# Kernel tuning notes

Measured on AMD Instinct MI355X. Metric: run time of the kernel, lower is better.

The kernel has to match this reference:

```python
import jax, jax.numpy as jnp
import numpy as np

N, E, DIN, HID, HEADS = 50000, 400000, 256, 64, 4
EPS_BN = 1e-5

def setup_inputs() -> dict:
    key = jax.random.key(0)
    ks = jax.random.split(key, 12)
    inp = {}
    inp['x'] = jax.random.normal(ks[0], (N, DIN), dtype=jnp.float32)
    inp['edge_index'] = jax.random.randint(ks[1], (2, E), 0, N, dtype=jnp.int64)
    s = 1.0 / np.sqrt(DIN)
    inp['W1'] = jax.random.uniform(ks[2], (DIN, HEADS * HID), jnp.float32, -s, s)
    inp['a_src1'] = jax.random.normal(ks[3], (HEADS, HID), dtype=jnp.float32) * 0.1
    inp['a_dst1'] = jax.random.normal(ks[4], (HEADS, HID), dtype=jnp.float32) * 0.1
    inp['b1'] = jnp.zeros((HEADS * HID,), jnp.float32)
    inp['bn1_w'] = jnp.ones((HEADS * HID,), jnp.float32)
    inp['bn1_b'] = jnp.zeros((HEADS * HID,), jnp.float32)
    inp['bn1_m'] = jnp.zeros((HEADS * HID,), jnp.float32)
    inp['bn1_v'] = jnp.ones((HEADS * HID,), jnp.float32)
    s2 = 1.0 / np.sqrt(HEADS * HID)
    inp['W2'] = jax.random.uniform(ks[5], (HEADS * HID, HID), jnp.float32, -s2, s2)
    inp['a_src2'] = jax.random.normal(ks[6], (1, HID), dtype=jnp.float32) * 0.1
    inp['a_dst2'] = jax.random.normal(ks[7], (1, HID), dtype=jnp.float32) * 0.1
    inp['b2'] = jnp.zeros((HID,), jnp.float32)
    inp['bn2_w'] = jnp.ones((HID,), jnp.float32)
    inp['bn2_b'] = jnp.zeros((HID,), jnp.float32)
    inp['bn2_m'] = jnp.zeros((HID,), jnp.float32)
    inp['bn2_v'] = jnp.ones((HID,), jnp.float32)
    sr = 1.0 / np.sqrt(HID)
    inp['Wr'] = jax.random.uniform(ks[8], (HID, 1), jnp.float32, -sr, sr)
    inp['br'] = jnp.zeros((1,), jnp.float32)
    inp['Wc'] = jax.random.uniform(ks[9], (HID, 1), jnp.float32, -sr, sr)
    inp['bc'] = jnp.zeros((1,), jnp.float32)
    return inp

def gat_layer(x, src, dst, W, a_src, a_dst, bias, concat):
    # x: [N, Fin] -> h: [N, H, D]
    H, D = a_src.shape
    h = (x @ W).reshape(-1, H, D)
    alpha_s = jnp.sum(h * a_src[None], axis=-1)  # [N, H]
    alpha_d = jnp.sum(h * a_dst[None], axis=-1)
    e = jax.nn.leaky_relu(alpha_s[src] + alpha_d[dst], 0.2)  # [Et, H]
    m = jax.ops.segment_max(e, dst, num_segments=N)
    m = jnp.where(jnp.isfinite(m), m, 0.0)
    ex = jnp.exp(e - m[dst])
    denom = jax.ops.segment_sum(ex, dst, num_segments=N)
    alpha = ex / (denom[dst] + 1e-16)  # segment softmax over incoming edges
    msg = h[src] * alpha[:, :, None]  # [Et, H, D]
    out = jax.ops.segment_sum(msg, dst, num_segments=N)  # [N, H, D]
    out = out.reshape(N, H * D) if concat else out.mean(axis=1)
    return out + bias

def batchnorm(x, w, b, mean, var):
    return (x - mean) * jax.lax.rsqrt(var + EPS_BN) * w + b

def reference(x, edge_index, W1, a_src1, a_dst1, b1, bn1_w, bn1_b, bn1_m, bn1_v,
              W2, a_src2, a_dst2, b2, bn2_w, bn2_b, bn2_m, bn2_v, Wr, br, Wc, bc):
    # add self loops (PyG GATConv default)
    loops = jnp.arange(N, dtype=edge_index.dtype)
    src = jnp.concatenate([edge_index[0], loops])
    dst = jnp.concatenate([edge_index[1], loops])
    h = gat_layer(x, src, dst, W1, a_src1, a_dst1, b1, concat=True)
    h = jax.nn.elu(batchnorm(h, bn1_w, bn1_b, bn1_m, bn1_v))
    h = gat_layer(h, src, dst, W2, a_src2, a_dst2, b2, concat=False)
    h = jax.nn.elu(batchnorm(h, bn2_w, bn2_b, bn2_m, bn2_v))
    reg = h @ Wr + br
    clf = jax.nn.sigmoid(h @ Wc + bc)
    return reg, clf
```

## Files before the change

kernel.cpp:

```cpp
#include <hip/hip_runtime.h>
#include <math.h>


typedef unsigned short ushort_t;
typedef unsigned char uchar_t;
typedef __attribute__((ext_vector_type(8))) unsigned short ushort8;
typedef __attribute__((ext_vector_type(4))) unsigned short ushort4v;
typedef __attribute__((ext_vector_type(8))) short short8;
typedef __attribute__((ext_vector_type(4))) float f32x4;
typedef __attribute__((ext_vector_type(2))) float f32x2;

#define EPS_BN 1e-5f

__device__ __forceinline__ ushort_t f2bf(float f) {
  unsigned u = __float_as_uint(f);
  unsigned r = u + 0x7fffu + ((u >> 16) & 1u);
  return (ushort_t)(r >> 16);
}
__device__ __forceinline__ float bf2f(ushort_t h) {
  return __uint_as_float((unsigned)h << 16);
}
__device__ __forceinline__ uchar_t f2fp8(float f) {
  return (uchar_t)(__builtin_amdgcn_cvt_pk_fp8_f32(f, f, 0, false) & 0xff);
}
__device__ __forceinline__ float leaky02(float x) { return x >= 0.f ? x : 0.2f * x; }
__device__ __forceinline__ float elu_fast(float x) {
  return x > 0.f ? x : __expf(x) - 1.f;
}
__device__ __forceinline__ float wave_sum(float v) {
#pragma unroll
  for (int o = 1; o < 64; o <<= 1) v += __shfl_xor(v, o, 64);
  return v;
}
__device__ __forceinline__ int wave_incl_scan(int v, int lane) {
#pragma unroll
  for (int off = 1; off < 64; off <<= 1) {
    int t = __shfl_up(v, off, 64);
    if (lane >= off) v += t;
  }
  return v;
}

__device__ __forceinline__ void gld_lds16(const ushort_t* g, ushort_t* l) {
  __builtin_amdgcn_global_load_lds(
      (const __attribute__((address_space(1))) unsigned int*)g,
      (__attribute__((address_space(3))) unsigned int*)l, 16, 0, 0);
}

__global__ __launch_bounds__(256) void hist_kernel(
    const int* __restrict__ dst, int* __restrict__ counts, int E) {
  int e = blockIdx.x * blockDim.x + threadIdx.x;
  if (e < E) atomicAdd(&counts[dst[e]], 1);
}

__global__ __launch_bounds__(256) void scan_chunks_kernel(
    const int* __restrict__ counts, int* __restrict__ offsets, int* __restrict__ partials,
    int N, int E, int* __restrict__ csr_src,
    const float* __restrict__ W1, const float* __restrict__ W2,
    ushort_t* __restrict__ W1t, ushort_t* __restrict__ W2t,
    const float* __restrict__ b1, const float* __restrict__ bn1w,
    const float* __restrict__ bn1b, const float* __restrict__ bn1m,
    const float* __restrict__ bn1v,
    const float* __restrict__ b2, const float* __restrict__ bn2w,
    const float* __restrict__ bn2b, const float* __restrict__ bn2m,
    const float* __restrict__ bn2v,
    float* __restrict__ S1, float* __restrict__ T1,
    float* __restrict__ S2, float* __restrict__ T2) {
  __shared__ int ws[4];
  const int tid = threadIdx.x, lane = tid & 63, wv = tid >> 6;
  const int i = blockIdx.x * 256 + tid;
  const int gsz = gridDim.x * 256;
  int v = (i < N) ? counts[i] : 0;
  int incl = wave_incl_scan(v, lane);
  if (lane == 63) ws[wv] = incl;
  __syncthreads();
  int wbase = 0;
  for (int k = 0; k < wv; ++k) wbase += ws[k];
  if (i < N) offsets[i] = wbase + incl - v;
  if (tid == 255) partials[blockIdx.x] = wbase + incl;

  for (int j = i; j < 256 * 256; j += gsz) {
    int k = j >> 8, n2 = j & 255;
    W1t[n2 * 256 + k] = f2bf(W1[j]);
  }
  for (int j = i; j < 256 * 64; j += gsz) {
    int k = j >> 6, n2 = j & 63;
    W2t[n2 * 256 + k] = f2bf(W2[j]);
  }
  if (i < 256) {
    float s = bn1w[i] * rsqrtf(bn1v[i] + EPS_BN);
    S1[i] = s;
    T1[i] = (b1[i] - bn1m[i]) * s + bn1b[i];
  } else if (i < 320) {
    int j = i - 256;
    float s = bn2w[j] * rsqrtf(bn2v[j] + EPS_BN);
    S2[j] = s;
    T2[j] = (b2[j] - bn2m[j]) * s + bn2b[j];
  } else if (i < 384) {
    csr_src[E + i - 320] = 0;
  }
}

__global__ __launch_bounds__(256) void scatter_kernel(
    const int* __restrict__ src, const int* __restrict__ dst,
    const int* __restrict__ offsets, const int* __restrict__ partials,
    int* __restrict__ cursor, int* __restrict__ csr_src,
    int* __restrict__ offs2, int E, int N, int nb) {
  __shared__ int pp[256];
  __shared__ int ws[4];
  __shared__ int tot;
  const int tid = threadIdx.x, lane = tid & 63, wv = tid >> 6;
  int v = (tid < nb) ? partials[tid] : 0;
  int incl = wave_incl_scan(v, lane);
  if (lane == 63) ws[wv] = incl;
  __syncthreads();
  int wbase = 0;
  for (int k = 0; k < wv; ++k) wbase += ws[k];
  pp[tid] = wbase + incl - v;
  if (tid == 255) tot = wbase + incl;
  __syncthreads();

  int idx = blockIdx.x * 256 + tid;
  if (idx < E) {
    int d = dst[idx];
    int p = atomicAdd(&cursor[d], 1);
    csr_src[offsets[d] + pp[d >> 8] + p] = src[idx];
  }
  if (idx <= N) {
    offs2[idx] = (idx < N) ? offsets[idx] + pp[idx >> 8] : tot;
  }
}

__global__ __launch_bounds__(512) void gemm1_persist(
    const float* __restrict__ X, const ushort_t* __restrict__ Bt,
    uchar_t* __restrict__ Cout, const float* __restrict__ avs,
    const float* __restrict__ avd,
    float* __restrict__ as_out, float* __restrict__ ad_out, int M, int ntiles) {
  __shared__ ushort_t Bs[256 * 256];
  __shared__ ushort_t As[32 * 256];
  const int t = threadIdx.x;
  const int w = t >> 6, l = t & 63;
  const int wr = w >> 2, wc = w & 3;

#pragma unroll
  for (int it = 0; it < 16; ++it) {
    int s = it * 512 + t;
    int i = s >> 5, sr = s & 31;
    int kb = sr >> 3, sl8 = sr & 7;
    int kc = (sl8 ^ (i & 7)) << 3;
    gld_lds16(Bt + (size_t)i * 256 + kb * 64 + kc, &Bs[s * 8]);
  }

  const int ar = t >> 4, k0a = (t & 15) * 16;
  int wd0, wd1;
  {
    int k = k0a;
    wd0 = ar * 256 + (k & ~63) + ((k & 63) ^ ((ar & 7) << 3));
    k = k0a + 8;
    wd1 = ar * 256 + (k & ~63) + ((k & 63) ^ ((ar & 7) << 3));
  }
  float4 fa0, fa1, fa2, fa3;
  {
    const float* src = X + (size_t)min(blockIdx.x * 32 + ar, M - 1) * 256 + k0a;
    fa0 = *(const float4*)(src);
    fa1 = *(const float4*)(src + 4);
    fa2 = *(const float4*)(src + 8);
    fa3 = *(const float4*)(src + 12);
  }

  const int fr = l & 15;
  const int kq = (l >> 4) << 3;
  const int fx = (fr & 7) << 3;
  const ushort_t* Ab = &As[(wr * 16 + fr) << 8];
  const ushort_t* Bb = &Bs[(wc * 64 + fr) << 8];

  float asw[4], adw[4];
#pragma unroll
  for (int j = 0; j < 4; ++j) {
    asw[j] = avs[wc * 64 + fr + j * 16];
    adw[j] = avd[wc * 64 + fr + j * 16];
  }

  for (int tile = blockIdx.x; tile < ntiles; tile += 256) {
    ushort8 u0, u1;
    u0[0] = f2bf(fa0.x); u0[1] = f2bf(fa0.y); u0[2] = f2bf(fa0.z); u0[3] = f2bf(fa0.w);
    u0[4] = f2bf(fa1.x); u0[5] = f2bf(fa1.y); u0[6] = f2bf(fa1.z); u0[7] = f2bf(fa1.w);
    u1[0] = f2bf(fa2.x); u1[1] = f2bf(fa2.y); u1[2] = f2bf(fa2.z); u1[3] = f2bf(fa2.w);
    u1[4] = f2bf(fa3.x); u1[5] = f2bf(fa3.y); u1[6] = f2bf(fa3.z); u1[7] = f2bf(fa3.w);
    __syncthreads();
    *(ushort8*)&As[wd0] = u0;
    *(ushort8*)&As[wd1] = u1;
    __syncthreads();

    {
      int nt_ = tile + 256;
      if (nt_ < ntiles) {
        const float* src = X + (size_t)min(nt_ * 32 + ar, M - 1) * 256 + k0a;
        fa0 = *(const float4*)(src);
        fa1 = *(const float4*)(src + 4);
        fa2 = *(const float4*)(src + 8);
        fa3 = *(const float4*)(src + 12);
      }
    }

    f32x4 acc[4];
#pragma unroll
    for (int j = 0; j < 4; ++j) acc[j] = (f32x4){0.f, 0.f, 0.f, 0.f};
#pragma unroll
    for (int k0 = 0; k0 < 256; k0 += 32) {
      const int kabs = k0 + kq;
      const int base = (kabs & ~63) + ((kabs & 63) ^ fx);
      short8 af = *(const short8*)&Ab[base];
#pragma unroll
      for (int j = 0; j < 4; ++j) {
        short8 bf8 = *(const short8*)&Bb[j * 4096 + base];
        acc[j] = __builtin_amdgcn_mfma_f32_16x16x32_bf16(af, bf8, acc[j], 0, 0, 0);
      }
    }

    const int rbase = tile * 32 + wr * 16 + (l >> 4) * 4;
#pragma unroll
    for (int j = 0; j < 4; ++j)
#pragma unroll
      for (int r4 = 0; r4 < 4; ++r4) {
        int row = rbase + r4;
        if (row < M)
          Cout[(size_t)row * 256 + wc * 64 + fr + j * 16] = f2fp8(acc[j][r4]);
      }

#pragma unroll
    for (int r4 = 0; r4 < 4; ++r4) {
      float s_ = acc[0][r4] * asw[0] + acc[1][r4] * asw[1] +
                 acc[2][r4] * asw[2] + acc[3][r4] * asw[3];
      float d_ = acc[0][r4] * adw[0] + acc[1][r4] * adw[1] +
                 acc[2][r4] * adw[2] + acc[3][r4] * adw[3];
#pragma unroll
      for (int o = 1; o < 16; o <<= 1) {
        s_ += __shfl_xor(s_, o, 64);
        d_ += __shfl_xor(d_, o, 64);
      }
      if ((l & 15) == 0) {
        int row = rbase + r4;
        if (row < M) {
          as_out[(size_t)row * 4 + wc] = s_;
          ad_out[(size_t)row * 4 + wc] = d_;
        }
      }
    }
  }
}

__global__ __launch_bounds__(256) void gemm2_fullk(
    const ushort_t* __restrict__ Ain, const ushort_t* __restrict__ Bt,
    ushort_t* __restrict__ Cout, const float* __restrict__ avs,
    const float* __restrict__ avd,
    float* __restrict__ as_out, float* __restrict__ ad_out, int M) {
  __shared__ ushort_t As[64 * 256];
  __shared__ ushort_t Bs[64 * 256];
  const int t = threadIdx.x;
  const int w = t >> 6, l = t & 63;
  const int m0 = blockIdx.x * 64;

  {
    const int slot = l & 7;
#pragma unroll
    for (int i = 0; i < 8; ++i) {
      const int r = w * 64 + i * 8 + (l >> 3);
      const int ir = r >> 2, kb = r & 3;
      const int kc = (slot ^ (ir & 7)) << 3;
      gld_lds16(Bt + (size_t)ir * 256 + kb * 64 + kc, &Bs[w * 4096 + i * 512]);
    }
#pragma unroll
    for (int i = 0; i < 8; ++i) {
      const int r = w * 64 + i * 8 + (l >> 3);
      const int ir = r >> 2, kb = r & 3;
      const int kc = (slot ^ (ir & 7)) << 3;
      const int arow = min(m0 + ir, M - 1);
      gld_lds16(Ain + (size_t)arow * 256 + kb * 64 + kc, &As[w * 4096 + i * 512]);
    }
  }
  asm volatile("s_waitcnt vmcnt(8)" ::: "memory");
  __builtin_amdgcn_s_barrier();
  asm volatile("s_waitcnt vmcnt(0)" ::: "memory");
  __builtin_amdgcn_sched_barrier(0);

  f32x4 acc[4];
#pragma unroll
  for (int j = 0; j < 4; ++j) acc[j] = (f32x4){0.f, 0.f, 0.f, 0.f};

  const int fr = l & 15;
  const int kq = (l >> 4) << 3;
  const int fx = (fr & 7) << 3;
  const ushort_t* Ab = &As[(w * 16 + fr) << 8];
  const ushort_t* Bb = &Bs[fr << 8];
#pragma unroll
  for (int k0 = 0; k0 < 256; k0 += 32) {
    const int kabs = k0 + kq;
    const int base = (kabs & ~63) + ((kabs & 63) ^ fx);
    short8 af = *(const short8*)&Ab[base];
#pragma unroll
    for (int j = 0; j < 4; ++j) {
      short8 bf8 = *(const short8*)&Bb[j * 4096 + base];
      acc[j] = __builtin_amdgcn_mfma_f32_16x16x32_bf16(af, bf8, acc[j], 0, 0, 0);
    }
  }

  const int rbase = m0 + w * 16 + (l >> 4) * 4;
#pragma unroll
  for (int j = 0; j < 4; ++j)
#pragma unroll
    for (int r4 = 0; r4 < 4; ++r4) {
      int row = rbase + r4;
      if (row < M)
        Cout[(size_t)row * 64 + fr + j * 16] = f2bf(acc[j][r4]);
    }

  float asw[4], adw[4];
#pragma unroll
  for (int j = 0; j < 4; ++j) {
    asw[j] = avs[fr + j * 16];
    adw[j] = avd[fr + j * 16];
  }
#pragma unroll
  for (int r4 = 0; r4 < 4; ++r4) {
    float s_ = acc[0][r4] * asw[0] + acc[1][r4] * asw[1] +
               acc[2][r4] * asw[2] + acc[3][r4] * asw[3];
    float d_ = acc[0][r4] * adw[0] + acc[1][r4] * adw[1] +
               acc[2][r4] * adw[2] + acc[3][r4] * adw[3];
#pragma unroll
    for (int o = 1; o < 16; o <<= 1) {
      s_ += __shfl_xor(s_, o, 64);
      d_ += __shfl_xor(d_, o, 64);
    }
    if ((l & 15) == 0) {
      int row = rbase + r4;
      if (row < M) {
        as_out[row] = s_;
        ad_out[row] = d_;
      }
    }
  }
}

__global__ __launch_bounds__(256) void agg1_kernel(
    const uchar_t* __restrict__ h1, const int* __restrict__ offsets,
    const int* __restrict__ csr, const float* __restrict__ as1,
    const float* __restrict__ ad1,
    const float* __restrict__ S1, const float* __restrict__ T1,
    ushort_t* __restrict__ out, int N) {
  __shared__ float ldsW[4][64][4];
  const int wv = threadIdx.x >> 6;
  int n = blockIdx.x * 4 + wv;
  int l = threadIdx.x & 63;
  if (n >= N) return;
  const int hh = l >> 4;
  int off = offsets[n], deg = offsets[n + 1] - off;
  const int* csrp = csr + off;
  const unsigned fb = (unsigned)l << 2;
  float4 adn = *(const float4*)&ad1[n * 4];
  float ad_h = (hh & 2) ? ((hh & 1) ? adn.w : adn.z) : ((hh & 1) ? adn.y : adn.x);

  f32x2 acc0 = {0.f, 0.f}, acc1 = {0.f, 0.f};
  float den = 0.f;

  for (int base = 0; base < deg; base += 64) {
    int cnt = min(64, deg - base);
    int s = 0;
    float4 w4 = make_float4(0.f, 0.f, 0.f, 0.f);
    if (l < cnt) {
      s = csrp[base + l];
      float4 a4 = *(const float4*)&as1[s * 4];
      w4.x = __expf(leaky02(a4.x + adn.x));
      w4.y = __expf(leaky02(a4.y + adn.y));
      w4.z = __expf(leaky02(a4.z + adn.z));
      w4.w = __expf(leaky02(a4.w + adn.w));
    }
    *(float4*)&ldsW[wv][l][0] = w4;
    for (int j = 0; j < cnt; j += 8) {
#pragma unroll
      for (int i = 0; i < 8; ++i) {
        int e = j + i;
        unsigned se = (unsigned)__builtin_amdgcn_readlane(s, e);
        float we = ldsW[wv][e][hh];
        unsigned q = *(const unsigned*)(h1 + (size_t)((se << 8) + fb));
        f32x2 lo = __builtin_amdgcn_cvt_pk_f32_fp8(q, false);
        f32x2 hi = __builtin_amdgcn_cvt_pk_f32_fp8(q, true);
        f32x2 w2 = {we, we};
        acc0 = lo * w2 + acc0;
        acc1 = hi * w2 + acc1;
        den += we;
      }
    }
  }

  float4 asn = *(const float4*)&as1[n * 4];
  float as_h = (hh & 2) ? ((hh & 1) ? asn.w : asn.z) : ((hh & 1) ? asn.y : asn.x);
  float ws = __expf(leaky02(as_h + ad_h));
  {
    unsigned q = *(const unsigned*)(h1 + (size_t)(((unsigned)n << 8) + fb));
    f32x2 lo = __builtin_amdgcn_cvt_pk_f32_fp8(q, false);
    f32x2 hi = __builtin_amdgcn_cvt_pk_f32_fp8(q, true);
    f32x2 w2 = {ws, ws};
    acc0 = lo * w2 + acc0;
    acc1 = hi * w2 + acc1;
  }
  float inv = 1.f / (den + ws + 1e-16f);

  const int c0 = l * 4;
  float4 Sv = *(const float4*)&S1[c0];
  float4 Tv = *(const float4*)&T1[c0];
  float o0 = fmaf(acc0.x, inv * Sv.x, Tv.x);
  float o1 = fmaf(acc0.y, inv * Sv.y, Tv.y);
  float o2 = fmaf(acc1.x, inv * Sv.z, Tv.z);
  float o3 = fmaf(acc1.y, inv * Sv.w, Tv.w);
  ushort4v o4;
  o4[0] = f2bf(elu_fast(o0));
  o4[1] = f2bf(elu_fast(o1));
  o4[2] = f2bf(elu_fast(o2));
  o4[3] = f2bf(elu_fast(o3));
  *(ushort4v*)&out[(size_t)n * 256 + c0] = o4;
}

__global__ __launch_bounds__(256) void agg2_kernel(
    const ushort_t* __restrict__ h2, const int* __restrict__ offsets,
    const int* __restrict__ csr, const float* __restrict__ as2,
    const float* __restrict__ ad2,
    const float* __restrict__ S2, const float* __restrict__ T2,
    const float* __restrict__ Wr, const float* __restrict__ br,
    const float* __restrict__ Wc, const float* __restrict__ bc,
    float* __restrict__ out_reg, float* __restrict__ out_clf, int N) {
  __shared__ float ldsW[4][64];
  __shared__ int ldsS[4][64];
  const int wv = threadIdx.x >> 6;
  int n = blockIdx.x * 4 + wv;
  int l = threadIdx.x & 63;
  if (n >= N) return;
  const int g = l >> 4, ll = l & 15;
  int off = offsets[n], deg = offsets[n + 1] - off;
  const int* csrp = csr + off;
  const size_t hoff = (size_t)ll * 4;
  float adn = ad2[n];

  float acc[4] = {0, 0, 0, 0};
  float ds = 0.f;

  for (int base = 0; base < deg; base += 64) {
    int cnt = min(64, deg - base);
    int s = 0;
    float wv_ = 0.f;
    if (l < cnt) {
      s = csrp[base + l];
      wv_ = __expf(leaky02(as2[s] + adn));
    }
    ldsS[wv][l] = s;
    ldsW[wv][l] = wv_;
    ds += wv_;
    for (int j = 0; j < cnt; j += 16) {
      int e0 = j + g, e1 = j + 4 + g, e2 = j + 8 + g, e3 = j + 12 + g;
      int s0 = ldsS[wv][e0], s1 = ldsS[wv][e1], s2 = ldsS[wv][e2], s3 = ldsS[wv][e3];
      float w0 = ldsW[wv][e0], w1 = ldsW[wv][e1], w2 = ldsW[wv][e2], w3 = ldsW[wv][e3];
      ushort4v r0 = *(const ushort4v*)&h2[(size_t)s0 * 64 + hoff];
      ushort4v r1 = *(const ushort4v*)&h2[(size_t)s1 * 64 + hoff];
      ushort4v r2 = *(const ushort4v*)&h2[(size_t)s2 * 64 + hoff];
      ushort4v r3 = *(const ushort4v*)&h2[(size_t)s3 * 64 + hoff];
#pragma unroll
      for (int k = 0; k < 4; ++k) acc[k] = fmaf(w0, bf2f(r0[k]), acc[k]);
#pragma unroll
      for (int k = 0; k < 4; ++k) acc[k] = fmaf(w1, bf2f(r1[k]), acc[k]);
#pragma unroll
      for (int k = 0; k < 4; ++k) acc[k] = fmaf(w2, bf2f(r2[k]), acc[k]);
#pragma unroll
      for (int k = 0; k < 4; ++k) acc[k] = fmaf(w3, bf2f(r3[k]), acc[k]);
    }
  }
#pragma unroll
  for (int k = 0; k < 4; ++k) {
    acc[k] += __shfl_xor(acc[k], 16, 64);
    acc[k] += __shfl_xor(acc[k], 32, 64);
  }
  float den = wave_sum(ds);
  float ws = __expf(leaky02(as2[n] + adn));
  ushort4v hn = *(const ushort4v*)&h2[(size_t)n * 64 + hoff];
#pragma unroll
  for (int k = 0; k < 4; ++k) acc[k] = fmaf(ws, bf2f(hn[k]), acc[k]);
  float inv = 1.f / (den + ws + 1e-16f);

  int c0 = ll * 4;
  float4 Sv = *(const float4*)&S2[c0];
  float4 Tv = *(const float4*)&T2[c0];
  float4 wr = *(const float4*)&Wr[c0];
  float4 wc = *(const float4*)&Wc[c0];
  float Sf[4] = {Sv.x, Sv.y, Sv.z, Sv.w};
  float Tf[4] = {Tv.x, Tv.y, Tv.z, Tv.w};
  float wrf[4] = {wr.x, wr.y, wr.z, wr.w};
  float wcf[4] = {wc.x, wc.y, wc.z, wc.w};
  float rs = 0.f, cs = 0.f;
#pragma unroll
  for (int q = 0; q < 4; ++q) {
    float o = fmaf(acc[q], inv * Sf[q], Tf[q]);
    o = elu_fast(o);
    rs = fmaf(o, wrf[q], rs);
    cs = fmaf(o, wcf[q], cs);
  }
#pragma unroll
  for (int o = 1; o < 16; o <<= 1) {
    rs += __shfl_xor(rs, o, 64);
    cs += __shfl_xor(cs, o, 64);
  }
  if (l == 0) {
    out_reg[n] = rs + br[0];
    float z = cs + bc[0];
    out_clf[n] = 1.f / (1.f + __expf(-z));
  }
}

extern "C" void kernel_launch(void* const* d_in, const int* in_sizes, int n_in,
                              void* d_out, int out_size, void* d_ws, size_t ws_size,
                              hipStream_t stream) {
  const float* x      = (const float*)d_in[0];
  const int*   ei     = (const int*)d_in[1];
  const float* W1     = (const float*)d_in[2];
  const float* a_src1 = (const float*)d_in[3];
  const float* a_dst1 = (const float*)d_in[4];
  const float* b1     = (const float*)d_in[5];
  const float* bn1w   = (const float*)d_in[6];
  const float* bn1b   = (const float*)d_in[7];
  const float* bn1m   = (const float*)d_in[8];
  const float* bn1v   = (const float*)d_in[9];
  const float* W2     = (const float*)d_in[10];
  const float* a_src2 = (const float*)d_in[11];
  const float* a_dst2 = (const float*)d_in[12];
  const float* b2     = (const float*)d_in[13];
  const float* bn2w   = (const float*)d_in[14];
  const float* bn2b   = (const float*)d_in[15];
  const float* bn2m   = (const float*)d_in[16];
  const float* bn2v   = (const float*)d_in[17];
  const float* Wr     = (const float*)d_in[18];
  const float* br     = (const float*)d_in[19];
  const float* Wc     = (const float*)d_in[20];
  const float* bc     = (const float*)d_in[21];

  const int N = in_sizes[0] / 256;
  const int E = in_sizes[1] / 2;
  const int* srcv = ei;
  const int* dstv = ei + E;

  char* w = (char*)d_ws;
  auto alloc = [&](size_t bytes) {
    char* p = w;
    w += (bytes + 255) & ~(size_t)255;
    return p;
  };
  const int nb = (N + 255) / 256;
  const size_t nbytes_rounded = ((size_t)N * 4 + 255) & ~(size_t)255;
  int* counts    = (int*)alloc((size_t)N * 4);
  int* cursor    = (int*)alloc((size_t)N * 4);
  int* offsets   = (int*)alloc((size_t)N * 4);
  int* offs2     = (int*)alloc((size_t)(N + 1) * 4);
  int* partials  = (int*)alloc((size_t)nb * 4);
  int* csr_src   = (int*)alloc((size_t)(E + 64) * 4);
  float* as1     = (float*)alloc((size_t)N * 4 * 4);
  float* ad1     = (float*)alloc((size_t)N * 4 * 4);
  float* as2     = (float*)alloc((size_t)N * 4);
  float* ad2     = (float*)alloc((size_t)N * 4);
  float* S1      = (float*)alloc(256 * 4);
  float* T1      = (float*)alloc(256 * 4);
  float* S2      = (float*)alloc(64 * 4);
  float* T2      = (float*)alloc(64 * 4);
  ushort_t* W1t  = (ushort_t*)alloc((size_t)256 * 256 * 2);
  ushort_t* W2t  = (ushort_t*)alloc((size_t)64 * 256 * 2);
  uchar_t* h1b   = (uchar_t*)alloc((size_t)N * 256);
  ushort_t* h1a  = (ushort_t*)alloc((size_t)N * 256 * 2);
  ushort_t* h2b  = (ushort_t*)alloc((size_t)N * 64 * 2);

  float* out_reg = (float*)d_out;

  hipMemsetAsync(counts, 0, nbytes_rounded * 2, stream);
  hist_kernel<<<(E + 255) / 256, 256, 0, stream>>>(dstv, counts, E);
  scan_chunks_kernel<<<nb, 256, 0, stream>>>(counts, offsets, partials, N, E, csr_src,
                                             W1, W2, W1t, W2t,
                                             b1, bn1w, bn1b, bn1m, bn1v,
                                             b2, bn2w, bn2b, bn2m, bn2v,
                                             S1, T1, S2, T2);
  {
    int items = max(E, N + 1);
    scatter_kernel<<<(items + 255) / 256, 256, 0, stream>>>(srcv, dstv, offsets, partials,
                                                            cursor, csr_src, offs2, E, N, nb);
  }

  const int nwb = (N + 3) / 4;
  const int ntiles1 = (N + 31) / 32;
  const int mtiles2 = (N + 63) / 64;

  gemm1_persist<<<256, 512, 0, stream>>>(
      x, W1t, h1b, a_src1, a_dst1, as1, ad1, N, ntiles1);
  agg1_kernel<<<nwb, 256, 0, stream>>>(h1b, offs2, csr_src, as1, ad1, S1, T1, h1a, N);

  gemm2_fullk<<<mtiles2, 256, 0, stream>>>(
      h1a, W2t, h2b, a_src2, a_dst2, as2, ad2, N);
  agg2_kernel<<<nwb, 256, 0, stream>>>(h2b, offs2, csr_src, as2, ad2, S2, T2,
                                       Wr, br, Wc, bc, out_reg, out_reg + N, N);
}
```

Measured before the change: 253.6 us.

## Process two nodes per wavefront in layer-2 aggregation with half-wave lanes

The layer-2 aggregation kernel now assigns each half-wave (32 lanes) its own destination node, so each lane holds two feature columns instead of four lanes per edge-group splitting 16 columns. Source indices and weights are packed into one float2 LDS array, and the inner loop walks all edges per half-wave with a 4-byte gather per lane. The aim is to cut cross-lane reductions and wasted lanes on low-degree nodes and to halve the block count. The cost is divergence: both halves loop to the larger of the two degrees, and each half-wave's loads are narrower per edge.

```diff
diff --git a/kernel.cpp b/kernel.cpp
--- a/kernel.cpp
+++ b/kernel.cpp
@@ -429,85 +429,73 @@
     const float* __restrict__ Wr, const float* __restrict__ br,
     const float* __restrict__ Wc, const float* __restrict__ bc,
     float* __restrict__ out_reg, float* __restrict__ out_clf, int N) {
-  __shared__ float ldsW[4][64];
-  __shared__ int ldsS[4][64];
+  __shared__ float2 ldsSW[4][64];
   const int wv = threadIdx.x >> 6;
-  int n = blockIdx.x * 4 + wv;
-  int l = threadIdx.x & 63;
-  if (n >= N) return;
-  const int g = l >> 4, ll = l & 15;
-  int off = offsets[n], deg = offsets[n + 1] - off;
+  const int l = threadIdx.x & 63;
+  const int h = l >> 5, q = l & 31;
+  int n = blockIdx.x * 8 + wv * 2 + h;
+  const bool valid = (n < N);
+  if (!valid) n = N - 1;
+  const int off = offsets[n], deg = offsets[n + 1] - off;
   const int* csrp = csr + off;
-  const size_t hoff = (size_t)ll * 4;
-  float adn = ad2[n];
-
-  float acc[4] = {0, 0, 0, 0};
-  float ds = 0.f;
-
-  for (int base = 0; base < deg; base += 64) {
-    int cnt = min(64, deg - base);
+  const float adn = ad2[n];
+  const int degw = max(deg, __shfl_xor(deg, 32, 64));
+
+  f32x2 acc = {0.f, 0.f};
+  float den = 0.f;
+  const int hb = h << 5;
+
+  for (int base = 0; base < degw; base += 32) {
     int s = 0;
-    float wv_ = 0.f;
-    if (l < cnt) {
-      s = csrp[base + l];
-      wv_ = __expf(leaky02(as2[s] + adn));
-    }
-    ldsS[wv][l] = s;
-    ldsW[wv][l] = wv_;
-    ds += wv_;
-    for (int j = 0; j < cnt; j += 16) {
-      int e0 = j + g, e1 = j + 4 + g, e2 = j + 8 + g, e3 = j + 12 + g;
-      int s0 = ldsS[wv][e0], s1 = ldsS[wv][e1], s2 = ldsS[wv][e2], s3 = ldsS[wv][e3];
-      float w0 = ldsW[wv][e0], w1 = ldsW[wv][e1], w2 = ldsW[wv][e2], w3 = ldsW[wv][e3];
-      ushort4v r0 = *(const ushort4v*)&h2[(size_t)s0 * 64 + hoff];
-      ushort4v r1 = *(const ushort4v*)&h2[(size_t)s1 * 64 + hoff];
-      ushort4v r2 = *(const ushort4v*)&h2[(size_t)s2 * 64 + hoff];
-      ushort4v r3 = *(const ushort4v*)&h2[(size_t)s3 * 64 + hoff];
-#pragma unroll
-      for (int k = 0; k < 4; ++k) acc[k] = fmaf(w0, bf2f(r0[k]), acc[k]);
-#pragma unroll
-      for (int k = 0; k < 4; ++k) acc[k] = fmaf(w1, bf2f(r1[k]), acc[k]);
-#pragma unroll
-      for (int k = 0; k < 4; ++k) acc[k] = fmaf(w2, bf2f(r2[k]), acc[k]);
-#pragma unroll
-      for (int k = 0; k < 4; ++k) acc[k] = fmaf(w3, bf2f(r3[k]), acc[k]);
-    }
-  }
-#pragma unroll
-  for (int k = 0; k < 4; ++k) {
-    acc[k] += __shfl_xor(acc[k], 16, 64);
-    acc[k] += __shfl_xor(acc[k], 32, 64);
-  }
-  float den = wave_sum(ds);
+    float w_ = 0.f;
+    int idx = base + q;
+    if (idx < deg) {
+      s = csrp[idx];
+      w_ = __expf(leaky02(as2[s] + adn));
+    }
+    float2 sw;
+    sw.x = __int_as_float(s);
+    sw.y = w_;
+    ldsSW[wv][l] = sw;
+    int cntw = min(32, degw - base);
+    for (int j = 0; j < cntw; j += 8) {
+#pragma unroll
+      for (int i = 0; i < 8; ++i) {
+        int e = j + i;
+        float2 t = ldsSW[wv][hb + e];
+        int se = __float_as_int(t.x);
+        float we = t.y;
+        unsigned d = *(const unsigned*)&h2[(size_t)se * 64 + (q << 1)];
+        acc.x = fmaf(we, bf2f((ushort_t)d), acc.x);
+        acc.y = fmaf(we, bf2f((ushort_t)(d >> 16)), acc.y);
+        den += we;
+      }
+    }
+  }
+
   float ws = __expf(leaky02(as2[n] + adn));
-  ushort4v hn = *(const ushort4v*)&h2[(size_t)n * 64 + hoff];
-#pragma unroll
-  for (int k = 0; k < 4; ++k) acc[k] = fmaf(ws, bf2f(hn[k]), acc[k]);
+  {
+    unsigned d = *(const unsigned*)&h2[(size_t)n * 64 + (q << 1)];
+    acc.x = fmaf(ws, bf2f((ushort_t)d), acc.x);
+    acc.y = fmaf(ws, bf2f((ushort_t)(d >> 16)), acc.y);
+  }
   float inv = 1.f / (den + ws + 1e-16f);
 
-  int c0 = ll * 4;
-  float4 Sv = *(const float4*)&S2[c0];
-  float4 Tv = *(const float4*)&T2[c0];
-  float4 wr = *(const float4*)&Wr[c0];
-  float4 wc = *(const float4*)&Wc[c0];
-  float Sf[4] = {Sv.x, Sv.y, Sv.z, Sv.w};
-  float Tf[4] = {Tv.x, Tv.y, Tv.z, Tv.w};
-  float wrf[4] = {wr.x, wr.y, wr.z, wr.w};
-  float wcf[4] = {wc.x, wc.y, wc.z, wc.w};
-  float rs = 0.f, cs = 0.f;
-#pragma unroll
-  for (int q = 0; q < 4; ++q) {
-    float o = fmaf(acc[q], inv * Sf[q], Tf[q]);
-    o = elu_fast(o);
-    rs = fmaf(o, wrf[q], rs);
-    cs = fmaf(o, wcf[q], cs);
-  }
-#pragma unroll
-  for (int o = 1; o < 16; o <<= 1) {
+  const int c0 = q << 1;
+  float2 Sv = *(const float2*)&S2[c0];
+  float2 Tv = *(const float2*)&T2[c0];
+  float2 wr = *(const float2*)&Wr[c0];
+  float2 wc = *(const float2*)&Wc[c0];
+  float o0 = elu_fast(fmaf(acc.x, inv * Sv.x, Tv.x));
+  float o1 = elu_fast(fmaf(acc.y, inv * Sv.y, Tv.y));
+  float rs = o0 * wr.x + o1 * wr.y;
+  float cs = o0 * wc.x + o1 * wc.y;
+#pragma unroll
+  for (int o = 1; o < 32; o <<= 1) {
     rs += __shfl_xor(rs, o, 64);
     cs += __shfl_xor(cs, o, 64);
   }
-  if (l == 0) {
+  if (q == 0 && valid) {
     out_reg[n] = rs + br[0];
     float z = cs + bc[0];
     out_clf[n] = 1.f / (1.f + __expf(-z));
@@ -589,6 +577,7 @@
   }
 
   const int nwb = (N + 3) / 4;
+  const int nwb2 = (N + 7) / 8;
   const int ntiles1 = (N + 31) / 32;
   const int mtiles2 = (N + 63) / 64;
 
@@ -598,6 +587,6 @@
 
   gemm2_fullk<<<mtiles2, 256, 0, stream>>>(
       h1a, W2t, h2b, a_src2, a_dst2, as2, ad2, N);
-  agg2_kernel<<<nwb, 256, 0, stream>>>(h2b, offs2, csr_src, as2, ad2, S2, T2,
-                                       Wr, br, Wc, bc, out_reg, out_reg + N, N);
-}
+  agg2_kernel<<<nwb2, 256, 0, stream>>>(h2b, offs2, csr_src, as2, ad2, S2, T2,
+                                        Wr, br, Wc, bc, out_reg, out_reg + N, N);
+}
```

Measured after the change: 242.1 us. 1.05x faster.
